# Kernel tuning notes

Hardware: AMD Instinct MI355X
Metric: run time of the kernel (lower is better)

Reference implementation:

```python
import jax, jax.numpy as jnp
import numpy as np

CANVAS_W = 1024.0
CANVAS_H = 1024.0
EPS = 1e-8
GOLDEN = 1.618
ALIGN_THRESH = 5.0


def _mse(p, t):
    return jnp.mean((p - t) ** 2)


def _smooth_l1(p, t):
    d = jnp.abs(p - t)
    return jnp.mean(jnp.where(d < 1.0, 0.5 * d * d, d - 0.5))


def setup_inputs() -> dict:
    key = jax.random.key(0)
    k1, k2, k3, k4 = jax.random.split(key, 4)
    B, N, D = 64, 256, 6
    return {
        "predicted_noise": jax.random.normal(k1, (B, N, D), dtype=jnp.float32),
        "target_noise": jax.random.normal(k2, (B, N, D), dtype=jnp.float32),
        "predicted_layout": jax.random.normal(k3, (B, N, D), dtype=jnp.float32),
        "target_layout": jax.random.normal(k4, (B, N, D), dtype=jnp.float32),
        "element_mask": jnp.ones((B, N), dtype=jnp.float32),
    }


def _iou_loss(pred, target):
    # boxes are (x, y, w, h)
    px1, py1 = pred[..., 0], pred[..., 1]
    px2, py2 = px1 + pred[..., 2], py1 + pred[..., 3]
    tx1, ty1 = target[..., 0], target[..., 1]
    tx2, ty2 = tx1 + target[..., 2], ty1 + target[..., 3]
    inter = jnp.maximum(jnp.minimum(px2, tx2) - jnp.maximum(px1, tx1), 0.0) * \
            jnp.maximum(jnp.minimum(py2, ty2) - jnp.maximum(py1, ty1), 0.0)
    pa = pred[..., 2] * pred[..., 3]
    ta = target[..., 2] * target[..., 3]
    iou = inter / (pa + ta - inter + EPS)
    return jnp.mean(1.0 - iou)


def _loss(predicted_noise, target_noise, predicted_layout, target_layout, element_mask):
    B, N, _ = predicted_noise.shape
    mask3 = element_mask[..., None]  # [B,N,1]
    pn = predicted_noise * mask3
    tn = target_noise * mask3
    pl = predicted_layout * mask3
    tl = target_layout * mask3

    npairs = N * (N - 1) / 2.0
    tri = jnp.triu(jnp.ones((N, N), dtype=pl.dtype), k=1)  # i<j pair mask
    pair_valid = element_mask[:, :, None] * element_mask[:, None, :]  # [B,N,N]

    # ---- noise loss (SmoothL1) ----
    noise_loss = _smooth_l1(pn, tn)

    # ---- position loss: MSE + 0.5*IoU ----
    position_loss = _mse(pl[..., :4], tl[..., :4]) + 0.5 * _iou_loss(pl[..., :4], tl[..., :4])

    # ---- layer loss: MSE + 0.3*pairwise ranking BCE ----
    p_layer, t_layer = pl[..., 4], tl[..., 4]
    diff = p_layer[:, None, :] - p_layer[:, :, None]          # [b,i,j] = p_j - p_i
    y = (t_layer[:, :, None] < t_layer[:, None, :]).astype(pl.dtype)
    # BCE(sigmoid(diff), y): -log sigmoid(d)=softplus(-d); torch clamps log terms at 100
    bce = y * jnp.minimum(jax.nn.softplus(-diff), 100.0) + \
          (1.0 - y) * jnp.minimum(jax.nn.softplus(diff), 100.0)
    ranking = jnp.sum(bce * tri) / (B * npairs)
    layer_loss = _mse(p_layer, t_layer) + 0.3 * ranking

    # ---- confidence loss ----
    confidence_loss = _mse(pl[..., 5], tl[..., 5])

    # ---- aesthetic loss ----
    aspect = pl[..., 2] / (pl[..., 3] + EPS)
    golden = jnp.mean(jnp.abs(aspect - GOLDEN))
    areas = pl[..., 2] * pl[..., 3] * element_mask
    size_harm = jnp.mean(jnp.std(areas, axis=1, ddof=1)) / (jnp.mean(areas) + EPS)
    cx = (pl[..., 0] + pl[..., 2] / 2) * element_mask
    cy = (pl[..., 1] + pl[..., 3] / 2) * element_mask
    valid_count = jnp.sum(element_mask, axis=1, keepdims=True)  # [B,1]
    # NOTE: faithful to original broadcasting ([B] / [B,1] -> [B,B])
    ocx = jnp.sum(cx, axis=1) / (valid_count + EPS)
    ocy = jnp.sum(cy, axis=1) / (valid_count + EPS)
    balance = jnp.mean(jnp.abs(ocx - CANVAS_W / 2) / (CANVAS_W / 2) +
                       jnp.abs(ocy - CANVAS_H / 2) / (CANVAS_H / 2))
    aesthetic_loss = 0.1 * golden + 0.2 * size_harm + 0.15 * balance

    # ---- overlap loss (pairwise) ----
    x1, y1, w, h = pl[..., 0], pl[..., 1], pl[..., 2], pl[..., 3]
    x2, y2 = x1 + w, y1 + h
    iw = jnp.maximum(jnp.minimum(x2[:, :, None], x2[:, None, :]) -
                     jnp.maximum(x1[:, :, None], x1[:, None, :]), 0.0)
    ih = jnp.maximum(jnp.minimum(y2[:, :, None], y2[:, None, :]) -
                     jnp.maximum(y1[:, :, None], y1[:, None, :]), 0.0)
    area = w * h
    min_area = jnp.minimum(area[:, :, None], area[:, None, :])
    overlap_ratio = (iw * ih) / (min_area + EPS) * pair_valid
    overlap_loss = jnp.sum(overlap_ratio * tri) / (B * npairs)

    # ---- alignment loss (6 edge types, pairwise) ----
    edges = jnp.stack([x1, x2, y1, y2, x1 + w / 2, y1 + h / 2], axis=0)  # [6,B,N]
    dist = jnp.abs(edges[:, :, :, None] - edges[:, :, None, :])          # [6,B,N,N]
    pen = jnp.where(dist < ALIGN_THRESH, dist / ALIGN_THRESH, 0.0) * pair_valid[None]
    alignment_loss = jnp.sum(pen * tri) / (B * 6.0 * npairs)

    total = (noise_loss + 1.0 * position_loss + 0.5 * layer_loss +
             0.3 * confidence_loss + 0.2 * aesthetic_loss +
             0.8 * overlap_loss + 0.4 * alignment_loss)
    return total


def reference(predicted_noise, target_noise, predicted_layout, target_layout, element_mask):
    return _loss(predicted_noise, target_noise, predicted_layout, target_layout, element_mask)
```

## Files before the change

kernel.cpp:

```cpp
#include <hip/hip_runtime.h>
#include <math.h>

#define NB 64
#define NN 256
#define NPAIRS 32640.0f
#define EPSF 1e-8f

#define PB(q) ((q) * 64)
#define PW(q) (704 + (q) * 256)

__device__ __forceinline__ float block_sum(float v, float* sred) {
    const int tid = threadIdx.x;
    #pragma unroll
    for (int off = 32; off > 0; off >>= 1) v += __shfl_down(v, off, 64);
    __syncthreads();
    if ((tid & 63) == 0) sred[tid >> 6] = v;
    __syncthreads();
    return sred[0] + sred[1] + sred[2] + sred[3];
}

__global__ __launch_bounds__(256) void loss_main(
    const float* __restrict__ pn, const float* __restrict__ tn,
    const float* __restrict__ pl, const float* __restrict__ tl,
    const float* __restrict__ mask, float* __restrict__ ws)
{
    __shared__ float sx1[NN], sy1[NN], sx2[NN], sy2[NN], scx[NN], scy[NN],
                     sar[NN], spl[NN], stl[NN], sm[NN];
    __shared__ float sred[4];

    const int b     = blockIdx.x >> 2;
    const int chunk = blockIdx.x & 3;
    const int i     = threadIdx.x;
    const int e     = b * NN + i;
    const float m   = mask[e];
    const int base  = e * 6;

    const float p0 = pl[base + 0] * m, p1 = pl[base + 1] * m,
                p2 = pl[base + 2] * m, p3 = pl[base + 3] * m,
                p4 = pl[base + 4] * m, p5 = pl[base + 5] * m;
    const float t0 = tl[base + 0] * m, t1 = tl[base + 1] * m,
                t2 = tl[base + 2] * m, t3 = tl[base + 3] * m,
                t4 = tl[base + 4] * m, t5 = tl[base + 5] * m;

    const float x2v = p0 + p2, y2v = p1 + p3;
    const float areav = p2 * p3;
    const float cxe = p0 + 0.5f * p2, cye = p1 + 0.5f * p3;

    sx1[i] = p0;  sy1[i] = p1;  sx2[i] = x2v;  sy2[i] = y2v;
    scx[i] = cxe; scy[i] = cye; sar[i] = areav;
    spl[i] = p4;  stl[i] = t4;  sm[i]  = m;
    __syncthreads();

    float noise = 0.f;
    #pragma unroll
    for (int k = 0; k < 6; ++k) {
        float d = fabsf(pn[base + k] * m - tn[base + k] * m);
        noise += (d < 1.f) ? 0.5f * d * d : d - 0.5f;
    }
    float posmse = (p0 - t0) * (p0 - t0) + (p1 - t1) * (p1 - t1)
                 + (p2 - t2) * (p2 - t2) + (p3 - t3) * (p3 - t3);
    const float tx2 = t0 + t2, ty2 = t1 + t3;
    float iw = fmaxf(fminf(x2v, tx2) - fmaxf(p0, t0), 0.f);
    float ih = fmaxf(fminf(y2v, ty2) - fmaxf(p1, t1), 0.f);
    float inter = iw * ih;
    float iouL = 1.f - inter / (p2 * p3 + t2 * t3 - inter + EPSF);
    float lmse = (p4 - t4) * (p4 - t4);
    float cmse = (p5 - t5) * (p5 - t5);
    float golden = fabsf(p2 / (p3 + EPSF) - 1.618f);
    float areaA = areav * m;
    float cxA = cxe * m, cyA = cye * m;

    float rank = 0.f, ovl = 0.f, aln = 0.f;
    const int dd0 = chunk * 32 + 1;
    for (int dd = dd0; dd < dd0 + 32; ++dd) {
        int j = (i + dd) & 255;
        if (dd == 128 && i >= 128) continue;
        float x1j = sx1[j], y1j = sy1[j], x2j = sx2[j], y2j = sy2[j];
        float cxj = scx[j], cyj = scy[j], arj = sar[j];
        float plj = spl[j], tlj = stl[j], mj = sm[j];
        float pv = m * mj;
        float ow = fmaxf(fminf(x2v, x2j) - fmaxf(p0, x1j), 0.f);
        float oh = fmaxf(fminf(y2v, y2j) - fmaxf(p1, y1j), 0.f);
        ovl += ow * oh / (fminf(areav, arj) + EPSF) * pv;
        float pen = 0.f, d;
        d = fabsf(p0  - x1j); pen += (d < 5.f) ? d : 0.f;
        d = fabsf(x2v - x2j); pen += (d < 5.f) ? d : 0.f;
        d = fabsf(p1  - y1j); pen += (d < 5.f) ? d : 0.f;
        d = fabsf(y2v - y2j); pen += (d < 5.f) ? d : 0.f;
        d = fabsf(cxe - cxj); pen += (d < 5.f) ? d : 0.f;
        d = fabsf(cye - cyj); pen += (d < 5.f) ? d : 0.f;
        aln += pen * 0.2f * pv;
        bool ilt = (i < j);
        float dlo = ilt ? (plj - p4) : (p4 - plj);
        float ylo = (ilt ? (t4 < tlj) : (tlj < t4)) ? 1.f : 0.f;
        float sp  = log1pf(expf(-fabsf(dlo)));
        float sp_pos = sp + fmaxf(dlo, 0.f);
        float sp_neg = sp + fmaxf(-dlo, 0.f);
        rank += ylo * fminf(sp_neg, 100.f) + (1.f - ylo) * fminf(sp_pos, 100.f);
    }

    float s;
    s = block_sum(noise,  sred); if (i == 0) ws[PB(0)  + b] = s;
    s = block_sum(posmse, sred); if (i == 0) ws[PB(1)  + b] = s;
    s = block_sum(iouL,   sred); if (i == 0) ws[PB(2)  + b] = s;
    s = block_sum(lmse,   sred); if (i == 0) ws[PB(3)  + b] = s;
    s = block_sum(cmse,   sred); if (i == 0) ws[PB(4)  + b] = s;
    s = block_sum(golden, sred); if (i == 0) ws[PB(5)  + b] = s;
    s = block_sum(areaA,  sred); if (i == 0) ws[PB(6)  + b] = s;
    s = block_sum(areaA * areaA, sred); if (i == 0) ws[PB(7) + b] = s;
    s = block_sum(cxA,    sred); if (i == 0) ws[PB(8)  + b] = s;
    s = block_sum(cyA,    sred); if (i == 0) ws[PB(9)  + b] = s;
    s = block_sum(m,      sred); if (i == 0) ws[PB(10) + b] = s;
    s = block_sum(rank, sred); if (i == 0) ws[PW(0) + blockIdx.x] = s;
    s = block_sum(ovl,  sred); if (i == 0) ws[PW(1) + blockIdx.x] = s;
    s = block_sum(aln,  sred); if (i == 0) ws[PW(2) + blockIdx.x] = s;
}

__global__ __launch_bounds__(256) void loss_final(
    const float* __restrict__ ws, float* __restrict__ out)
{
    __shared__ float sred[4];
    __shared__ float bcx[NB], bcy[NB], bvc[NB];
    const int t = threadIdx.x;

    float v_noise = 0.f, v_pos = 0.f, v_iou = 0.f, v_lm = 0.f, v_cf = 0.f,
          v_go = 0.f, v_ar = 0.f, v_std = 0.f;
    if (t < NB) {
        v_noise = ws[PB(0) + t];
        v_pos   = ws[PB(1) + t];
        v_iou   = ws[PB(2) + t];
        v_lm    = ws[PB(3) + t];
        v_cf    = ws[PB(4) + t];
        v_go    = ws[PB(5) + t];
        v_ar    = ws[PB(6) + t];
        float a2 = ws[PB(7) + t];
        float var = (a2 - v_ar * v_ar * (1.f / 256.f)) * (1.f / 255.f);
        v_std = sqrtf(fmaxf(var, 0.f));
        bcx[t] = ws[PB(8) + t];
        bcy[t] = ws[PB(9) + t];
        bvc[t] = ws[PB(10) + t];
    }
    float v_rank = ws[PW(0) + t];
    float v_ovl  = ws[PW(1) + t];
    float v_aln  = ws[PW(2) + t];
    __syncthreads();

    float v_bal = 0.f;
    if (t < NB) {
        float inv = 1.f / (bvc[t] + EPSF);
        for (int j = 0; j < NB; ++j) {
            v_bal += fabsf(bcx[j] * inv - 512.f) * (1.f / 512.f)
                   + fabsf(bcy[j] * inv - 512.f) * (1.f / 512.f);
        }
    }

    float S_noise = block_sum(v_noise, sred);
    float S_pos   = block_sum(v_pos,   sred);
    float S_iou   = block_sum(v_iou,   sred);
    float S_lm    = block_sum(v_lm,    sred);
    float S_cf    = block_sum(v_cf,    sred);
    float S_go    = block_sum(v_go,    sred);
    float S_ar    = block_sum(v_ar,    sred);
    float S_std   = block_sum(v_std,   sred);
    float S_bal   = block_sum(v_bal,   sred);
    float S_rank  = block_sum(v_rank,  sred);
    float S_ovl   = block_sum(v_ovl,   sred);
    float S_aln   = block_sum(v_aln,   sred);

    if (t == 0) {
        const float BN = 64.f * 256.f;
        float noise_loss = S_noise / (BN * 6.f);
        float position   = S_pos / (BN * 4.f) + 0.5f * (S_iou / BN);
        float layer      = S_lm / BN + 0.3f * (S_rank / (64.f * NPAIRS));
        float conf       = S_cf / BN;
        float golden     = S_go / BN;
        float size_harm  = (S_std / 64.f) / (S_ar / BN + EPSF);
        float balance    = S_bal / 4096.f;
        float aes        = 0.1f * golden + 0.2f * size_harm + 0.15f * balance;
        float ovl        = S_ovl / (64.f * NPAIRS);
        float aln        = S_aln / (64.f * 6.f * NPAIRS);
        out[0] = noise_loss + position + 0.5f * layer + 0.3f * conf
               + 0.2f * aes + 0.8f * ovl + 0.4f * aln;
    }
}

extern "C" void kernel_launch(void* const* d_in, const int* in_sizes, int n_in,
                              void* d_out, int out_size, void* d_ws, size_t ws_size,
                              hipStream_t stream) {
    const float* pn   = (const float*)d_in[0];
    const float* tn   = (const float*)d_in[1];
    const float* pl   = (const float*)d_in[2];
    const float* tl   = (const float*)d_in[3];
    const float* mask = (const float*)d_in[4];
    float* ws  = (float*)d_ws;
    float* out = (float*)d_out;
    hipLaunchKernelGGL(loss_main, dim3(256), dim3(256), 0, stream,
                       pn, tn, pl, tl, mask, ws);
    hipLaunchKernelGGL(loss_final, dim3(1), dim3(256), 0, stream, ws, out);
}
```

Measured before the change: 85.42 us.

## Pack shared arrays into float4, split per-batch reductions across chunks, fast math

Packs the ten per-element shared arrays into two float4 and one float2 array so each pairwise iteration issues three wide LDS loads instead of ten scalar ones. Replaces log1pf/expf with __logf/__expf, unrolls the pair loop by four, and loads inputs as float2. The eleven per-batch reductions, which every chunk block used to compute redundantly, are now split so each of the four chunk blocks does only a subset. This removes redundant reduction barriers and global loads, at the cost of slightly lower precision in the softplus term.

Result: faster. 75.86 us (-11.2%).

```diff
diff --git a/kernel.cpp b/kernel.cpp
--- a/kernel.cpp
+++ b/kernel.cpp
@@ -24,8 +24,8 @@
     const float* __restrict__ pl, const float* __restrict__ tl,
     const float* __restrict__ mask, float* __restrict__ ws)
 {
-    __shared__ float sx1[NN], sy1[NN], sx2[NN], sy2[NN], scx[NN], scy[NN],
-                     sar[NN], spl[NN], stl[NN], sm[NN];
+    __shared__ float4 sA[NN], sB[NN];
+    __shared__ float2 sC[NN];
     __shared__ float sred[4];
 
     const int b     = blockIdx.x >> 2;
@@ -33,87 +33,104 @@
     const int i     = threadIdx.x;
     const int e     = b * NN + i;
     const float m   = mask[e];
-    const int base  = e * 6;
-
-    const float p0 = pl[base + 0] * m, p1 = pl[base + 1] * m,
-                p2 = pl[base + 2] * m, p3 = pl[base + 3] * m,
-                p4 = pl[base + 4] * m, p5 = pl[base + 5] * m;
-    const float t0 = tl[base + 0] * m, t1 = tl[base + 1] * m,
-                t2 = tl[base + 2] * m, t3 = tl[base + 3] * m,
-                t4 = tl[base + 4] * m, t5 = tl[base + 5] * m;
+
+    const float2* pl2 = (const float2*)pl;
+    const float2* tl2 = (const float2*)tl;
+    const int r2 = e * 3;
+    const float2 pla = pl2[r2 + 0], plb = pl2[r2 + 1], plc = pl2[r2 + 2];
+    const float2 tlc = tl2[r2 + 2];
+
+    const float p0 = pla.x * m, p1 = pla.y * m,
+                p2 = plb.x * m, p3 = plb.y * m,
+                p4 = plc.x * m, p5 = plc.y * m;
+    const float t4 = tlc.x * m, t5 = tlc.y * m;
 
     const float x2v = p0 + p2, y2v = p1 + p3;
     const float areav = p2 * p3;
     const float cxe = p0 + 0.5f * p2, cye = p1 + 0.5f * p3;
 
-    sx1[i] = p0;  sy1[i] = p1;  sx2[i] = x2v;  sy2[i] = y2v;
-    scx[i] = cxe; scy[i] = cye; sar[i] = areav;
-    spl[i] = p4;  stl[i] = t4;  sm[i]  = m;
-    __syncthreads();
-
-    float noise = 0.f;
-    #pragma unroll
-    for (int k = 0; k < 6; ++k) {
-        float d = fabsf(pn[base + k] * m - tn[base + k] * m);
-        noise += (d < 1.f) ? 0.5f * d * d : d - 0.5f;
-    }
-    float posmse = (p0 - t0) * (p0 - t0) + (p1 - t1) * (p1 - t1)
-                 + (p2 - t2) * (p2 - t2) + (p3 - t3) * (p3 - t3);
-    const float tx2 = t0 + t2, ty2 = t1 + t3;
-    float iw = fmaxf(fminf(x2v, tx2) - fmaxf(p0, t0), 0.f);
-    float ih = fmaxf(fminf(y2v, ty2) - fmaxf(p1, t1), 0.f);
-    float inter = iw * ih;
-    float iouL = 1.f - inter / (p2 * p3 + t2 * t3 - inter + EPSF);
-    float lmse = (p4 - t4) * (p4 - t4);
-    float cmse = (p5 - t5) * (p5 - t5);
-    float golden = fabsf(p2 / (p3 + EPSF) - 1.618f);
-    float areaA = areav * m;
-    float cxA = cxe * m, cyA = cye * m;
+    sA[i] = make_float4(p0, p1, x2v, y2v);
+    sB[i] = make_float4(cxe, cye, areav, p4);
+    sC[i] = make_float2(t4, m);
+    __syncthreads();
 
     float rank = 0.f, ovl = 0.f, aln = 0.f;
     const int dd0 = chunk * 32 + 1;
+    #pragma unroll 4
     for (int dd = dd0; dd < dd0 + 32; ++dd) {
         int j = (i + dd) & 255;
         if (dd == 128 && i >= 128) continue;
-        float x1j = sx1[j], y1j = sy1[j], x2j = sx2[j], y2j = sy2[j];
-        float cxj = scx[j], cyj = scy[j], arj = sar[j];
-        float plj = spl[j], tlj = stl[j], mj = sm[j];
-        float pv = m * mj;
-        float ow = fmaxf(fminf(x2v, x2j) - fmaxf(p0, x1j), 0.f);
-        float oh = fmaxf(fminf(y2v, y2j) - fmaxf(p1, y1j), 0.f);
-        ovl += ow * oh / (fminf(areav, arj) + EPSF) * pv;
+        float4 aj = sA[j];
+        float4 bj = sB[j];
+        float2 cj = sC[j];
+        float pv = m * cj.y;
+        float ow = fmaxf(fminf(x2v, aj.z) - fmaxf(p0, aj.x), 0.f);
+        float oh = fmaxf(fminf(y2v, aj.w) - fmaxf(p1, aj.y), 0.f);
+        ovl += ow * oh / (fminf(areav, bj.z) + EPSF) * pv;
         float pen = 0.f, d;
-        d = fabsf(p0  - x1j); pen += (d < 5.f) ? d : 0.f;
-        d = fabsf(x2v - x2j); pen += (d < 5.f) ? d : 0.f;
-        d = fabsf(p1  - y1j); pen += (d < 5.f) ? d : 0.f;
-        d = fabsf(y2v - y2j); pen += (d < 5.f) ? d : 0.f;
-        d = fabsf(cxe - cxj); pen += (d < 5.f) ? d : 0.f;
-        d = fabsf(cye - cyj); pen += (d < 5.f) ? d : 0.f;
+        d = fabsf(p0  - aj.x); pen += (d < 5.f) ? d : 0.f;
+        d = fabsf(x2v - aj.z); pen += (d < 5.f) ? d : 0.f;
+        d = fabsf(p1  - aj.y); pen += (d < 5.f) ? d : 0.f;
+        d = fabsf(y2v - aj.w); pen += (d < 5.f) ? d : 0.f;
+        d = fabsf(cxe - bj.x); pen += (d < 5.f) ? d : 0.f;
+        d = fabsf(cye - bj.y); pen += (d < 5.f) ? d : 0.f;
         aln += pen * 0.2f * pv;
         bool ilt = (i < j);
-        float dlo = ilt ? (plj - p4) : (p4 - plj);
-        float ylo = (ilt ? (t4 < tlj) : (tlj < t4)) ? 1.f : 0.f;
-        float sp  = log1pf(expf(-fabsf(dlo)));
+        float dlo = ilt ? (bj.w - p4) : (p4 - bj.w);
+        float ylo = (ilt ? (t4 < cj.x) : (cj.x < t4)) ? 1.f : 0.f;
+        float sp  = __logf(1.f + __expf(-fabsf(dlo)));
         float sp_pos = sp + fmaxf(dlo, 0.f);
         float sp_neg = sp + fmaxf(-dlo, 0.f);
         rank += ylo * fminf(sp_neg, 100.f) + (1.f - ylo) * fminf(sp_pos, 100.f);
     }
 
     float s;
-    s = block_sum(noise,  sred); if (i == 0) ws[PB(0)  + b] = s;
-    s = block_sum(posmse, sred); if (i == 0) ws[PB(1)  + b] = s;
-    s = block_sum(iouL,   sred); if (i == 0) ws[PB(2)  + b] = s;
-    s = block_sum(lmse,   sred); if (i == 0) ws[PB(3)  + b] = s;
-    s = block_sum(cmse,   sred); if (i == 0) ws[PB(4)  + b] = s;
-    s = block_sum(golden, sred); if (i == 0) ws[PB(5)  + b] = s;
-    s = block_sum(areaA,  sred); if (i == 0) ws[PB(6)  + b] = s;
-    s = block_sum(areaA * areaA, sred); if (i == 0) ws[PB(7) + b] = s;
-    s = block_sum(cxA,    sred); if (i == 0) ws[PB(8)  + b] = s;
-    s = block_sum(cyA,    sred); if (i == 0) ws[PB(9)  + b] = s;
-    s = block_sum(m,      sred); if (i == 0) ws[PB(10) + b] = s;
     s = block_sum(rank, sred); if (i == 0) ws[PW(0) + blockIdx.x] = s;
     s = block_sum(ovl,  sred); if (i == 0) ws[PW(1) + blockIdx.x] = s;
     s = block_sum(aln,  sred); if (i == 0) ws[PW(2) + blockIdx.x] = s;
+
+    if (chunk == 0) {
+        const float2* pn2 = (const float2*)pn;
+        const float2* tn2 = (const float2*)tn;
+        float noise = 0.f;
+        #pragma unroll
+        for (int k = 0; k < 3; ++k) {
+            float2 a = pn2[r2 + k], bb = tn2[r2 + k];
+            float d0 = fabsf(a.x * m - bb.x * m);
+            float d1 = fabsf(a.y * m - bb.y * m);
+            noise += (d0 < 1.f) ? 0.5f * d0 * d0 : d0 - 0.5f;
+            noise += (d1 < 1.f) ? 0.5f * d1 * d1 : d1 - 0.5f;
+        }
+        s = block_sum(noise, sred); if (i == 0) ws[PB(0) + b] = s;
+    } else if (chunk == 1) {
+        const float2 tla = tl2[r2 + 0], tlb = tl2[r2 + 1];
+        const float t0 = tla.x * m, t1 = tla.y * m,
+                    t2 = tlb.x * m, t3 = tlb.y * m;
+        float posmse = (p0 - t0) * (p0 - t0) + (p1 - t1) * (p1 - t1)
+                     + (p2 - t2) * (p2 - t2) + (p3 - t3) * (p3 - t3);
+        const float tx2 = t0 + t2, ty2 = t1 + t3;
+        float iw = fmaxf(fminf(x2v, tx2) - fmaxf(p0, t0), 0.f);
+        float ih = fmaxf(fminf(y2v, ty2) - fmaxf(p1, t1), 0.f);
+        float inter = iw * ih;
+        float iouL = 1.f - inter / (areav + t2 * t3 - inter + EPSF);
+        float lmse = (p4 - t4) * (p4 - t4);
+        float cmse = (p5 - t5) * (p5 - t5);
+        s = block_sum(posmse, sred); if (i == 0) ws[PB(1) + b] = s;
+        s = block_sum(iouL,   sred); if (i == 0) ws[PB(2) + b] = s;
+        s = block_sum(lmse,   sred); if (i == 0) ws[PB(3) + b] = s;
+        s = block_sum(cmse,   sred); if (i == 0) ws[PB(4) + b] = s;
+    } else if (chunk == 2) {
+        float golden = fabsf(p2 / (p3 + EPSF) - 1.618f);
+        float areaA  = areav * m;
+        s = block_sum(golden, sred);        if (i == 0) ws[PB(5) + b] = s;
+        s = block_sum(areaA,  sred);        if (i == 0) ws[PB(6) + b] = s;
+        s = block_sum(areaA * areaA, sred); if (i == 0) ws[PB(7) + b] = s;
+    } else {
+        float cxA = cxe * m, cyA = cye * m;
+        s = block_sum(cxA, sred); if (i == 0) ws[PB(8)  + b] = s;
+        s = block_sum(cyA, sred); if (i == 0) ws[PB(9)  + b] = s;
+        s = block_sum(m,   sred); if (i == 0) ws[PB(10) + b] = s;
+    }
 }
 
 __global__ __launch_bounds__(256) void loss_final(
```
